# Kernel optimization log

Hardware: AMD Instinct MI355X
Metric: run time of the kernel (lower is better)

Reference implementation:

```python
import jax, jax.numpy as jnp
import numpy as np

EPS = 1e-5

def _ln(x, g, b):
    mu = x.mean(-1, keepdims=True)
    var = ((x - mu) ** 2).mean(-1, keepdims=True)
    return (x - mu) / jnp.sqrt(var + EPS) * g + b


def setup_inputs() -> dict:
    key = jax.random.key(0)
    B, Hd, Wd = 4, 32, 32
    C, heads = 1024, 16
    N = Hd * Wd
    pd = (C // 4) // 4  # DynamicPosBias pos_dim = 64
    hid = 4 * C
    ks = jax.random.split(key, 24)

    def w(k, shape):
        return jax.random.normal(k, shape, jnp.float32) * 0.02

    inp = {
        'x': jax.random.normal(ks[0], (B, N, C), jnp.float32),
        'norm1_g': jnp.ones((C,), jnp.float32), 'norm1_b': jnp.zeros((C,), jnp.float32),
        'q_w': w(ks[1], (C, C)),              # no bias (qkv_bias=False)
        'kv_w': w(ks[2], (C, 2 * C)),
        'proj_w': w(ks[3], (C, C)), 'proj_b': jnp.zeros((C,), jnp.float32),
        'pos_proj_w': w(ks[4], (2, pd)), 'pos_proj_b': jnp.zeros((pd,), jnp.float32),
        'ln1_g': jnp.ones((pd,), jnp.float32), 'ln1_b': jnp.zeros((pd,), jnp.float32),
        'lin1_w': w(ks[5], (pd, pd)), 'lin1_b': jnp.zeros((pd,), jnp.float32),
        'ln2_g': jnp.ones((pd,), jnp.float32), 'ln2_b': jnp.zeros((pd,), jnp.float32),
        'lin2_w': w(ks[6], (pd, pd)), 'lin2_b': jnp.zeros((pd,), jnp.float32),
        'ln3_g': jnp.ones((pd,), jnp.float32), 'ln3_b': jnp.zeros((pd,), jnp.float32),
        'lin3_w': w(ks[7], (pd, heads)), 'lin3_b': jnp.zeros((heads,), jnp.float32),
        'norm2_g': jnp.ones((C,), jnp.float32), 'norm2_b': jnp.zeros((C,), jnp.float32),
        'fc1_w': w(ks[8], (C, hid)), 'fc1_b': jnp.zeros((hid,), jnp.float32),
        'fc2_w': w(ks[9], (hid, C)), 'fc2_b': jnp.zeros((C,), jnp.float32),
        'H': Hd, 'W': Wd,
    }
    return inp


def _rel_pos(H, W):
    # coordinate offsets fed to the bias MLP: [(2H-1)(2W-1), 2]
    ph = np.arange(1 - H, H)
    pw = np.arange(1 - W, W)
    bh, bw = np.meshgrid(ph, pw, indexing='ij')
    biases = np.stack([bh.ravel(), bw.ravel()], axis=1).astype(np.float32)
    # relative position index: [HW, HW]
    ch, cw = np.meshgrid(np.arange(H), np.arange(W), indexing='ij')
    flat = np.stack([ch.ravel(), cw.ravel()])                 # [2, HW]
    rel = flat[:, :, None] - flat[:, None, :]                 # [2, HW, HW]
    rel = rel.transpose(1, 2, 0)
    rel[:, :, 0] += H - 1
    rel[:, :, 1] += W - 1
    rel[:, :, 0] *= 2 * W - 1
    idx = rel.sum(-1)                                         # [HW, HW]
    return jnp.asarray(biases), jnp.asarray(idx)


def reference(x, norm1_g, norm1_b, q_w, kv_w, proj_w, proj_b,
              pos_proj_w, pos_proj_b, ln1_g, ln1_b, lin1_w, lin1_b,
              ln2_g, ln2_b, lin2_w, lin2_b, ln3_g, ln3_b, lin3_w, lin3_b,
              norm2_g, norm2_b, fc1_w, fc1_b, fc2_w, fc2_b, H, W):
    B, N, C = x.shape
    heads = lin3_w.shape[1]
    d = C // heads
    scale = d ** (-0.5)

    # --- HLGAttention (stage_index==4: group_size=(H,W), h0_token=None) ---
    xn = _ln(x, norm1_g, norm1_b)
    q = (xn @ q_w).reshape(B, N, heads, d).transpose(0, 2, 1, 3)   # [B,h,N,d]
    kv = (xn @ kv_w).reshape(B, N, 2, heads, d)
    k = kv[:, :, 0].transpose(0, 2, 1, 3)                          # [B,h,N,d]
    v = kv[:, :, 1].transpose(0, 2, 1, 3)
    attn = jnp.einsum('bhnd,bhmd->bhnm', q, k) * scale

    # dynamic relative position bias via small MLP + gather
    biases, rel_idx = _rel_pos(H, W)
    pos = biases @ pos_proj_w + pos_proj_b
    pos = jax.nn.relu(_ln(pos, ln1_g, ln1_b)) @ lin1_w + lin1_b
    pos = jax.nn.relu(_ln(pos, ln2_g, ln2_b)) @ lin2_w + lin2_b
    pos = jax.nn.relu(_ln(pos, ln3_g, ln3_b)) @ lin3_w + lin3_b    # [(2H-1)(2W-1), heads]
    rpb = pos[rel_idx]                                              # [N,N,heads]
    attn = attn + rpb.transpose(2, 0, 1)[None]

    attn = jax.nn.softmax(attn, axis=-1)
    out = jnp.einsum('bhnm,bhmd->bhnd', attn, v)
    out = out.transpose(0, 2, 1, 3).reshape(B, N, C)
    out = out @ proj_w + proj_b
    x = x + out

    # --- MLP block ---
    h = _ln(x, norm2_g, norm2_b) @ fc1_w + fc1_b
    h = jax.nn.gelu(h, approximate=False)
    x = x + (h @ fc2_w + fc2_b)
    return x
```

## Files before the change

kernel.cpp:

```cpp
#include <hip/hip_runtime.h>
#include <cstdint>
#include <cstddef>

typedef __attribute__((ext_vector_type(8))) __bf16 bf16x8;
typedef __attribute__((ext_vector_type(8))) unsigned short us8;
typedef __attribute__((ext_vector_type(4))) unsigned short us4;
typedef __attribute__((ext_vector_type(4))) float f32x4;
typedef __attribute__((ext_vector_type(16))) float f32x16;

#define DEVI static __device__ __forceinline__

DEVI unsigned short f2bf(float f) {
  union { float f; unsigned u; } v; v.f = f;
  unsigned r = v.u + 0x7fffu + ((v.u >> 16) & 1u);
  return (unsigned short)(r >> 16);
}

DEVI f32x4 mfma16(us8 a, us8 b, f32x4 c) {
  return __builtin_amdgcn_mfma_f32_16x16x32_bf16(
      __builtin_bit_cast(bf16x8, a), __builtin_bit_cast(bf16x8, b), c, 0, 0, 0);
}

DEVI f32x16 mfma32(us8 a, us8 b, f32x16 c) {
  return __builtin_amdgcn_mfma_f32_32x32x16_bf16(
      __builtin_bit_cast(bf16x8, a), __builtin_bit_cast(bf16x8, b), c, 0, 0, 0);
}

DEVI f32x4 fzero4() { f32x4 v = {0.f, 0.f, 0.f, 0.f}; return v; }

DEVI float gelu_f(float v) {
  float z = 0.7978845608f * v * (1.f + 0.044715f * v * v);
  float e = __expf(2.f * z);
  float r = 1.f / (e + 1.f);
  return v * (1.f - r);
}

DEVI unsigned pkbf(float lo, float hi) {
  unsigned r;
  asm("v_cvt_pk_bf16_f32 %0, %1, %2" : "=v"(r) : "v"(lo), "v"(hi));
  return r;
}

DEVI void pswap(unsigned& x, unsigned& y) {
  asm volatile("v_permlane32_swap_b32 %0, %1" : "+v"(x), "+v"(y));
}

DEVI void gload16(const unsigned short* g, unsigned short* l) {
  __builtin_amdgcn_global_load_lds(
      (const __attribute__((address_space(1))) unsigned int*)g,
      (__attribute__((address_space(3))) unsigned int*)l, 16, 0, 0);
}

__global__ __launch_bounds__(256)
void transpose_w(const float* __restrict__ w, unsigned short* __restrict__ wt,
                 int K, int N) {
  __shared__ unsigned short tile[64][65];
  const int t = threadIdx.x;
  const int kb = blockIdx.x * 64, nb = blockIdx.y * 64;
#pragma unroll
  for (int i = 0; i < 4; ++i) {
    int r = i * 16 + (t >> 4);
    int c = (t & 15) * 4;
    float4 v = *(const float4*)(w + (size_t)(kb + r) * N + nb + c);
    tile[r][c + 0] = f2bf(v.x);
    tile[r][c + 1] = f2bf(v.y);
    tile[r][c + 2] = f2bf(v.z);
    tile[r][c + 3] = f2bf(v.w);
  }
  __syncthreads();
#pragma unroll
  for (int i = 0; i < 4; ++i) {
    int n = i * 16 + (t >> 4);
    int k = (t & 15) * 4;
    us4 o;
    o[0] = tile[k + 0][n];
    o[1] = tile[k + 1][n];
    o[2] = tile[k + 2][n];
    o[3] = tile[k + 3][n];
    *(us4*)(wt + (size_t)(nb + n) * K + kb + k) = o;
  }
}

__global__ __launch_bounds__(256)
void ln_kernel(const float* __restrict__ x, const float* __restrict__ g,
               const float* __restrict__ b, unsigned short* __restrict__ o) {
  const int row = blockIdx.x;
  const int tid = threadIdx.x;
  const float* xr = x + (size_t)row * 1024;
  float4 v = *(const float4*)(xr + tid * 4);
  float s = v.x + v.y + v.z + v.w;
  float sq = v.x * v.x + v.y * v.y + v.z * v.z + v.w * v.w;
#pragma unroll
  for (int m = 1; m < 64; m <<= 1) {
    s += __shfl_xor(s, m, 64);
    sq += __shfl_xor(sq, m, 64);
  }
  __shared__ float ss[4], ssq[4];
  const int wid = tid >> 6, lane = tid & 63;
  if (lane == 0) { ss[wid] = s; ssq[wid] = sq; }
  __syncthreads();
  s = ss[0] + ss[1] + ss[2] + ss[3];
  sq = ssq[0] + ssq[1] + ssq[2] + ssq[3];
  const float mu = s * (1.f / 1024.f);
  const float var = sq * (1.f / 1024.f) - mu * mu;
  const float rstd = rsqrtf(var + 1e-5f);
  const int c = tid * 4;
  float4 gv = *(const float4*)(g + c);
  float4 bv = *(const float4*)(b + c);
  us4 ov;
  ov[0] = f2bf((v.x - mu) * rstd * gv.x + bv.x);
  ov[1] = f2bf((v.y - mu) * rstd * gv.y + bv.y);
  ov[2] = f2bf((v.z - mu) * rstd * gv.z + bv.z);
  ov[3] = f2bf((v.w - mu) * rstd * gv.w + bv.w);
  *(us4*)(o + (size_t)row * 1024 + c) = ov;
}

DEVI float pos_layer(float p, const float* __restrict__ g,
                     const float* __restrict__ be, const float* __restrict__ w,
                     const float* __restrict__ bb, int lane) {
  float s = p, sq = p * p;
#pragma unroll
  for (int m = 1; m < 64; m <<= 1) {
    s += __shfl_xor(s, m, 64);
    sq += __shfl_xor(sq, m, 64);
  }
  float mu = s * (1.f / 64.f);
  float var = sq * (1.f / 64.f) - mu * mu;
  float rstd = rsqrtf(var + 1e-5f);
  float y = fmaxf((p - mu) * rstd * g[lane] + be[lane], 0.f);
  float o = bb[lane];
  for (int k = 0; k < 64; ++k) {
    float yk = __shfl(y, k, 64);
    o += yk * w[k * 64 + lane];
  }
  return o;
}

__global__ __launch_bounds__(256)
void pos_mlp(const float* __restrict__ pp_w, const float* __restrict__ pp_b,
             const float* __restrict__ g1, const float* __restrict__ b1,
             const float* __restrict__ w1, const float* __restrict__ bb1,
             const float* __restrict__ g2, const float* __restrict__ b2,
             const float* __restrict__ w2, const float* __restrict__ bb2,
             const float* __restrict__ g3, const float* __restrict__ b3,
             const float* __restrict__ w3, const float* __restrict__ bb3,
             float* __restrict__ posT) {
  const int wid = threadIdx.x >> 6, lane = threadIdx.x & 63;
  const int row = blockIdx.x * 4 + wid;
  if (row >= 3969) return;
  const float bh = (float)(row / 63) - 31.f;
  const float bw = (float)(row % 63) - 31.f;
  float p = bh * pp_w[lane] + bw * pp_w[64 + lane] + pp_b[lane];
  p = pos_layer(p, g1, b1, w1, bb1, lane);
  p = pos_layer(p, g2, b2, w2, bb2, lane);
  float s = p, sq = p * p;
#pragma unroll
  for (int m = 1; m < 64; m <<= 1) {
    s += __shfl_xor(s, m, 64);
    sq += __shfl_xor(sq, m, 64);
  }
  float mu = s * (1.f / 64.f);
  float var = sq * (1.f / 64.f) - mu * mu;
  float rstd = rsqrtf(var + 1e-5f);
  float y = fmaxf((p - mu) * rstd * g3[lane] + b3[lane], 0.f);
  float o = 0.f;
  for (int k = 0; k < 64; ++k) {
    float yk = __shfl(y, k, 64);
    o += yk * w3[k * 16 + (lane & 15)];
  }
  if (lane < 16) posT[(size_t)lane * 3969 + row] = o + bb3[lane];
}

template <int BM, int BN, bool HAS_BIAS, bool GELU_, bool HAS_RES,
          bool OUT_BF16, bool OUT_F32>
__global__ __launch_bounds__(256)
void gemm_bt(const unsigned short* __restrict__ A,
             const unsigned short* __restrict__ Bt,
             const float* __restrict__ bias, const float* __restrict__ res,
             unsigned short* __restrict__ outb, float* __restrict__ outf,
             int M, int N, int K) {
  constexpr int MT = BM / 32;
  constexpr int NT = BN / 32;
  __shared__ unsigned short As[BM * 128];
  __shared__ unsigned short Bs[BN * 128];
  const int tid = threadIdx.x;
  const int lane = tid & 63;
  const int wid = tid >> 6;
  const int lr = lane & 15, lg = lane >> 4;
  const int wr = wid >> 1, wc = wid & 1;
  const int brow = blockIdx.x, bcol = blockIdx.y;

  f32x4 acc[MT][NT];
#pragma unroll
  for (int mt = 0; mt < MT; ++mt)
#pragma unroll
    for (int nt = 0; nt < NT; ++nt) acc[mt][nt] = fzero4();

  const int sr = wid * 4 + (lane >> 4);
  const int sc = ((lane & 15) ^ ((sr & 7) << 1)) * 8;
  const unsigned short* Ag = A + (size_t)(brow * BM + sr) * K + sc;
  const unsigned short* Bg = Bt + (size_t)(bcol * BN + sr) * K + sc;

  const int nkb = K >> 7;
  for (int kb = 0; kb < nkb; ++kb) {
    __syncthreads();
#pragma unroll
    for (int q = 0; q < BM / 16; ++q)
      gload16(Ag + (size_t)(q * 16) * K + kb * 128,
              As + (q * 16 + wid * 4) * 128);
#pragma unroll
    for (int q = 0; q < BN / 16; ++q)
      gload16(Bg + (size_t)(q * 16) * K + kb * 128,
              Bs + (q * 16 + wid * 4) * 128);
    __syncthreads();
#pragma unroll
    for (int ks = 0; ks < 4; ++ks) {
      us8 af[MT], bfr[NT];
#pragma unroll
      for (int mt = 0; mt < MT; ++mt) {
        const int r = wr * (BM / 2) + mt * 16 + lr;
        const int ck = (ks * 4 + lg) ^ ((r & 7) << 1);
        af[mt] = *(const us8*)((const char*)As + r * 256 + ck * 16);
      }
#pragma unroll
      for (int nt = 0; nt < NT; ++nt) {
        const int r = wc * (BN / 2) + nt * 16 + lr;
        const int ck = (ks * 4 + lg) ^ ((r & 7) << 1);
        bfr[nt] = *(const us8*)((const char*)Bs + r * 256 + ck * 16);
      }
      __builtin_amdgcn_s_setprio(1);
#pragma unroll
      for (int mt = 0; mt < MT; ++mt)
#pragma unroll
        for (int nt = 0; nt < NT; ++nt)
          acc[mt][nt] = mfma16(af[mt], bfr[nt], acc[mt][nt]);
      __builtin_amdgcn_s_setprio(0);
    }
  }

#pragma unroll
  for (int mt = 0; mt < MT; ++mt) {
    const int row = brow * BM + wr * (BM / 2) + mt * 16 + 4 * lg;
#pragma unroll
    for (int nt = 0; nt < NT; ++nt) {
      const int col = bcol * BN + wc * (BN / 2) + nt * 16 + lr;
      float bsv = 0.f;
      if constexpr (HAS_BIAS) bsv = bias[col];
#pragma unroll
      for (int i = 0; i < 4; ++i) {
        float v = acc[mt][nt][i] + bsv;
        if constexpr (GELU_) v = gelu_f(v);
        if constexpr (HAS_RES) v += res[(size_t)(row + i) * N + col];
        if constexpr (OUT_F32) outf[(size_t)(row + i) * N + col] = v;
        if constexpr (OUT_BF16) outb[(size_t)(row + i) * N + col] = f2bf(v);
      }
    }
  }
}

__global__ __launch_bounds__(256)
void attn_kernel(const unsigned short* __restrict__ qkv,
                 const float* __restrict__ posT,
                 unsigned short* __restrict__ attnb) {
  __shared__ unsigned short Ks[64 * 64];
  __shared__ unsigned short Vt[64 * 64];

  const int tid = threadIdx.x;
  const int wid = tid >> 6;
  const int lane = tid & 63;
  const int ql = lane & 31;
  const int hi = lane >> 5;

  const int p = blockIdx.x;
  const int orig = (p & 7) * 64 + (p >> 3);
  const int b = orig >> 7;
  const int h = (orig >> 3) & 15;
  const int qt = orig & 7;

  const int LDQ = 3072;
  const int qg = qt * 128 + wid * 32 + ql;

  us8 qf[4];
  const unsigned short* qptr =
      qkv + (size_t)(b * 1024 + qg) * LDQ + h * 64 + 8 * hi;
#pragma unroll
  for (int db = 0; db < 4; ++db) qf[db] = *(const us8*)(qptr + db * 16);

  const float* pb = posT + (size_t)h * 3969;
  const int rb_q = ((qg >> 5) + 31) * 63 + (qg & 31) + 31 - 4 * hi;

  f32x16 oacc[2];
#pragma unroll
  for (int r = 0; r < 16; ++r) { oacc[0][r] = 0.f; oacc[1][r] = 0.f; }
  float mreg = -1e30f, lsum = 0.f;

  const int ksr = tid >> 2;
  const int ksc = (tid & 3) * 16;
  const int vk0 = (tid >> 4) * 4;
  const int vd0 = (tid & 15) * 4;

  const unsigned short* kbase = qkv + (size_t)(b * 1024) * LDQ + 1024 + h * 64;
  const unsigned short* vbase = qkv + (size_t)(b * 1024) * LDQ + 2048 + h * 64;

  us8 pk0 = *(const us8*)(kbase + (size_t)ksr * LDQ + ksc);
  us8 pk1 = *(const us8*)(kbase + (size_t)ksr * LDQ + ksc + 8);
  us4 pvv[4];
#pragma unroll
  for (int j = 0; j < 4; ++j)
    pvv[j] = *(const us4*)(vbase + (size_t)(vk0 + j) * LDQ + vd0);

  for (int kt = 0; kt < 16; ++kt) {
    __syncthreads();
    {
      char* ksb = (char*)Ks;
      const int swr = (ksr & 7) << 4;
      *(us8*)(ksb + ksr * 128 + ((ksc * 2) ^ swr)) = pk0;
      *(us8*)(ksb + ksr * 128 + (((ksc + 8) * 2) ^ swr)) = pk1;
      char* vtb = (char*)Vt;
#pragma unroll
      for (int u = 0; u < 4; ++u) {
        us4 w;
        w[0] = pvv[0][u]; w[1] = pvv[1][u]; w[2] = pvv[2][u]; w[3] = pvv[3][u];
        const int d = vd0 + u;
        *(us4*)(vtb + d * 128 + ((vk0 * 2) ^ ((d & 7) << 4))) = w;
      }
    }
    __syncthreads();

    if (kt < 15) {
      const unsigned short* kb2 = kbase + (size_t)((kt + 1) * 64) * LDQ;
      const unsigned short* vb2 = vbase + (size_t)((kt + 1) * 64) * LDQ;
      pk0 = *(const us8*)(kb2 + (size_t)ksr * LDQ + ksc);
      pk1 = *(const us8*)(kb2 + (size_t)ksr * LDQ + ksc + 8);
#pragma unroll
      for (int j = 0; j < 4; ++j)
        pvv[j] = *(const us4*)(vb2 + (size_t)(vk0 + j) * LDQ + vd0);
    }

    f32x16 st0, st1;
#pragma unroll
    for (int r = 0; r < 16; ++r) { st0[r] = 0.f; st1[r] = 0.f; }
    const char* ksb = (const char*)Ks;
    const int kswz = (ql & 7) << 4;
    __builtin_amdgcn_s_setprio(1);
#pragma unroll
    for (int db = 0; db < 4; ++db) {
      const int coff = (db * 32 + 16 * hi) ^ kswz;
      us8 kf0 = *(const us8*)(ksb + ql * 128 + coff);
      us8 kf1 = *(const us8*)(ksb + (32 + ql) * 128 + coff);
      st0 = mfma32(kf0, qf[db], st0);
      st1 = mfma32(kf1, qf[db], st1);
    }
    __builtin_amdgcn_s_setprio(0);

    float sv0[16], sv1[16];
    const float* pb0 = pb + (rb_q - 63 * (2 * kt));
    const float* pb1 = pb0 - 63;
    float mm[16];
#pragma unroll
    for (int r = 0; r < 16; ++r) {
      const int roff = (r & 3) + 8 * (r >> 2);
      float a = st0[r] * 0.125f + pb0[-roff];
      float c = st1[r] * 0.125f + pb1[-roff];
      sv0[r] = a;
      sv1[r] = c;
      mm[r] = fmaxf(a, c);
    }
#pragma unroll
    for (int w = 8; w >= 1; w >>= 1)
#pragma unroll
      for (int r = 0; r < w; ++r) mm[r] = fmaxf(mm[r], mm[r + w]);
    float mx = fmaxf(mreg, mm[0]);
    mx = fmaxf(mx, __shfl_xor(mx, 32, 64));
    const float f = __expf(mreg - mx);
    mreg = mx;

    float ts[16];
#pragma unroll
    for (int r = 0; r < 16; ++r) {
      float e0 = __expf(sv0[r] - mx);
      float e1 = __expf(sv1[r] - mx);
      sv0[r] = e0;
      sv1[r] = e1;
      ts[r] = e0 + e1;
    }
#pragma unroll
    for (int w = 8; w >= 1; w >>= 1)
#pragma unroll
      for (int r = 0; r < w; ++r) ts[r] += ts[r + w];
    lsum = lsum * f + ts[0];
#pragma unroll
    for (int r = 0; r < 16; ++r) { oacc[0][r] *= f; oacc[1][r] *= f; }

    const char* vtb = (const char*)Vt;
    auto pvfrag = [&](const float* sv, int kb) {
      const int B0 = (kb & 1) * 8;
      unsigned a0 = pkbf(sv[B0 + 0], sv[B0 + 1]);
      unsigned a1 = pkbf(sv[B0 + 2], sv[B0 + 3]);
      unsigned b0 = pkbf(sv[B0 + 4], sv[B0 + 5]);
      unsigned b1 = pkbf(sv[B0 + 6], sv[B0 + 7]);
      pswap(a0, b0);
      pswap(a1, b1);
      union { us8 s; unsigned u[4]; } fu;
      fu.u[0] = a0; fu.u[1] = a1; fu.u[2] = b0; fu.u[3] = b1;
      const int coff = (kb * 32 + 16 * hi) ^ kswz;
      us8 vf0 = *(const us8*)(vtb + ql * 128 + coff);
      us8 vf1 = *(const us8*)(vtb + (32 + ql) * 128 + coff);
      __builtin_amdgcn_s_setprio(1);
      oacc[0] = mfma32(vf0, fu.s, oacc[0]);
      oacc[1] = mfma32(vf1, fu.s, oacc[1]);
      __builtin_amdgcn_s_setprio(0);
    };
    pvfrag(sv0, 0);
    pvfrag(sv0, 1);
    pvfrag(sv1, 2);
    pvfrag(sv1, 3);
  }

  lsum += __shfl_xor(lsum, 32, 64);
  const float inv = 1.f / lsum;
  unsigned short* orow = attnb + (size_t)(b * 1024 + qg) * 1024 + h * 64;
#pragma unroll
  for (int dm = 0; dm < 2; ++dm)
#pragma unroll
    for (int r = 0; r < 16; ++r) {
      const int d = dm * 32 + (r & 3) + 8 * (r >> 2) + 4 * hi;
      orow[d] = f2bf(oacc[dm][r] * inv);
    }
}

extern "C" void kernel_launch(void* const* d_in, const int* in_sizes, int n_in,
                              void* d_out, int out_size, void* d_ws,
                              size_t ws_size, hipStream_t stream) {
  const float* x = (const float*)d_in[0];
  const float* n1g = (const float*)d_in[1];
  const float* n1b = (const float*)d_in[2];
  const float* q_w = (const float*)d_in[3];
  const float* kv_w = (const float*)d_in[4];
  const float* proj_w = (const float*)d_in[5];
  const float* proj_b = (const float*)d_in[6];
  const float* pp_w = (const float*)d_in[7];
  const float* pp_b = (const float*)d_in[8];
  const float* ln1g = (const float*)d_in[9];
  const float* ln1b = (const float*)d_in[10];
  const float* lin1w = (const float*)d_in[11];
  const float* lin1b = (const float*)d_in[12];
  const float* ln2g = (const float*)d_in[13];
  const float* ln2b = (const float*)d_in[14];
  const float* lin2w = (const float*)d_in[15];
  const float* lin2b = (const float*)d_in[16];
  const float* ln3g = (const float*)d_in[17];
  const float* ln3b = (const float*)d_in[18];
  const float* lin3w = (const float*)d_in[19];
  const float* lin3b = (const float*)d_in[20];
  const float* n2g = (const float*)d_in[21];
  const float* n2b = (const float*)d_in[22];
  const float* fc1_w = (const float*)d_in[23];
  const float* fc1_b = (const float*)d_in[24];
  const float* fc2_w = (const float*)d_in[25];
  const float* fc2_b = (const float*)d_in[26];
  float* out = (float*)d_out;

  char* ws = (char*)d_ws;
  const size_t MB = 1024ull * 1024ull;
  unsigned short* qkvT = (unsigned short*)(ws + 0 * MB);
  unsigned short* projT = (unsigned short*)(ws + 6 * MB);
  unsigned short* fc1T = (unsigned short*)(ws + 8 * MB);
  unsigned short* fc2T = (unsigned short*)(ws + 16 * MB);
  unsigned short* xn = (unsigned short*)(ws + 24 * MB);
  unsigned short* qkv = (unsigned short*)(ws + 32 * MB);
  unsigned short* attnb = (unsigned short*)(ws + 56 * MB);
  float* x1 = (float*)(ws + 64 * MB);
  unsigned short* x2n = (unsigned short*)(ws + 80 * MB);
  unsigned short* hb = (unsigned short*)(ws + 88 * MB);
  float* posT = (float*)(ws + 120 * MB);

  transpose_w<<<dim3(16, 16), 256, 0, stream>>>(q_w, qkvT, 1024, 1024);
  transpose_w<<<dim3(16, 32), 256, 0, stream>>>(
      kv_w, qkvT + (size_t)1024 * 1024, 1024, 2048);
  transpose_w<<<dim3(16, 16), 256, 0, stream>>>(proj_w, projT, 1024, 1024);
  transpose_w<<<dim3(16, 64), 256, 0, stream>>>(fc1_w, fc1T, 1024, 4096);
  transpose_w<<<dim3(64, 16), 256, 0, stream>>>(fc2_w, fc2T, 4096, 1024);

  ln_kernel<<<4096, 256, 0, stream>>>(x, n1g, n1b, xn);
  pos_mlp<<<993, 256, 0, stream>>>(pp_w, pp_b, ln1g, ln1b, lin1w, lin1b, ln2g,
                                   ln2b, lin2w, lin2b, ln3g, ln3b, lin3w,
                                   lin3b, posT);

  gemm_bt<128, 128, false, false, false, true, false>
      <<<dim3(32, 24), 256, 0, stream>>>(xn, qkvT, nullptr, nullptr, qkv,
                                         nullptr, 4096, 3072, 1024);

  attn_kernel<<<512, 256, 0, stream>>>(qkv, posT, attnb);

  gemm_bt<64, 128, true, false, true, false, true>
      <<<dim3(64, 8), 256, 0, stream>>>(attnb, projT, proj_b, x, nullptr, x1,
                                        4096, 1024, 1024);

  ln_kernel<<<4096, 256, 0, stream>>>(x1, n2g, n2b, x2n);

  gemm_bt<128, 128, true, true, false, true, false>
      <<<dim3(32, 32), 256, 0, stream>>>(x2n, fc1T, fc1_b, nullptr, hb,
                                         nullptr, 4096, 4096, 1024);

  gemm_bt<64, 128, true, false, true, false, true>
      <<<dim3(64, 8), 256, 0, stream>>>(hb, fc2T, fc2_b, x1, nullptr, out,
                                        4096, 1024, 4096);

  (void)in_sizes; (void)n_in; (void)out_size; (void)ws_size;
}
```

Measured before the change: 239.7 us.

## Fuse prep kernels, halve attention block size, add lazy softmax rescaling

Merges the five weight-transpose launches, the first LayerNorm and the position-bias MLP into a single block-indexed prep kernel, removing several kernel launches. The attention kernel now uses 128-thread blocks covering 64 query rows each, launched as 1024 blocks with wider per-thread K/V staging loads. Online softmax now rescales the accumulator only when the new row max exceeds the running max by more than 8, which skips exp and multiply work but lets unnormalised exponentials grow up to e^8.

After: 223.4 us, median of 2. 1.07x faster.

```diff
diff --git a/kernel.cpp b/kernel.cpp
--- a/kernel.cpp
+++ b/kernel.cpp
@@ -51,12 +51,11 @@
       (__attribute__((address_space(3))) unsigned int*)l, 16, 0, 0);
 }
 
-__global__ __launch_bounds__(256)
-void transpose_w(const float* __restrict__ w, unsigned short* __restrict__ wt,
-                 int K, int N) {
-  __shared__ unsigned short tile[64][65];
+DEVI void transpose_body(const float* __restrict__ w,
+                         unsigned short* __restrict__ wt, int K, int N,
+                         int kbi, int nbi, unsigned short (*tile)[65]) {
   const int t = threadIdx.x;
-  const int kb = blockIdx.x * 64, nb = blockIdx.y * 64;
+  const int kb = kbi * 64, nb = nbi * 64;
 #pragma unroll
   for (int i = 0; i < 4; ++i) {
     int r = i * 16 + (t >> 4);
@@ -78,6 +77,123 @@
     o[2] = tile[k + 2][n];
     o[3] = tile[k + 3][n];
     *(us4*)(wt + (size_t)(nb + n) * K + kb + k) = o;
+  }
+}
+
+DEVI float pos_layer(float p, const float* __restrict__ g,
+                     const float* __restrict__ be, const float* __restrict__ w,
+                     const float* __restrict__ bb, int lane) {
+  float s = p, sq = p * p;
+#pragma unroll
+  for (int m = 1; m < 64; m <<= 1) {
+    s += __shfl_xor(s, m, 64);
+    sq += __shfl_xor(sq, m, 64);
+  }
+  float mu = s * (1.f / 64.f);
+  float var = sq * (1.f / 64.f) - mu * mu;
+  float rstd = rsqrtf(var + 1e-5f);
+  float y = fmaxf((p - mu) * rstd * g[lane] + be[lane], 0.f);
+  float o = bb[lane];
+  for (int k = 0; k < 64; ++k) {
+    float yk = __shfl(y, k, 64);
+    o += yk * w[k * 64 + lane];
+  }
+  return o;
+}
+
+__global__ __launch_bounds__(256)
+void prep_kernel(const float* __restrict__ x, const float* __restrict__ n1g,
+                 const float* __restrict__ n1b, unsigned short* __restrict__ xn,
+                 const float* __restrict__ q_w, const float* __restrict__ kv_w,
+                 const float* __restrict__ proj_w,
+                 const float* __restrict__ fc1_w,
+                 const float* __restrict__ fc2_w,
+                 unsigned short* __restrict__ qkvT,
+                 unsigned short* __restrict__ projT,
+                 unsigned short* __restrict__ fc1T,
+                 unsigned short* __restrict__ fc2T,
+                 const float* __restrict__ pp_w, const float* __restrict__ pp_b,
+                 const float* __restrict__ g1, const float* __restrict__ b1,
+                 const float* __restrict__ w1, const float* __restrict__ bb1,
+                 const float* __restrict__ g2, const float* __restrict__ b2,
+                 const float* __restrict__ w2, const float* __restrict__ bb2,
+                 const float* __restrict__ g3, const float* __restrict__ b3,
+                 const float* __restrict__ w3, const float* __restrict__ bb3,
+                 float* __restrict__ posT) {
+  __shared__ unsigned short tile[64][65];
+  __shared__ float ss[4], ssq[4];
+  const int blk = blockIdx.x;
+  const int tid = threadIdx.x;
+
+  if (blk < 4096) {
+    const int row = blk;
+    const float* xr = x + (size_t)row * 1024;
+    float4 v = *(const float4*)(xr + tid * 4);
+    float s = v.x + v.y + v.z + v.w;
+    float sq = v.x * v.x + v.y * v.y + v.z * v.z + v.w * v.w;
+#pragma unroll
+    for (int m = 1; m < 64; m <<= 1) {
+      s += __shfl_xor(s, m, 64);
+      sq += __shfl_xor(sq, m, 64);
+    }
+    const int wid = tid >> 6, lane = tid & 63;
+    if (lane == 0) { ss[wid] = s; ssq[wid] = sq; }
+    __syncthreads();
+    s = ss[0] + ss[1] + ss[2] + ss[3];
+    sq = ssq[0] + ssq[1] + ssq[2] + ssq[3];
+    const float mu = s * (1.f / 1024.f);
+    const float var = sq * (1.f / 1024.f) - mu * mu;
+    const float rstd = rsqrtf(var + 1e-5f);
+    const int c = tid * 4;
+    float4 gv = *(const float4*)(n1g + c);
+    float4 bv = *(const float4*)(n1b + c);
+    us4 ov;
+    ov[0] = f2bf((v.x - mu) * rstd * gv.x + bv.x);
+    ov[1] = f2bf((v.y - mu) * rstd * gv.y + bv.y);
+    ov[2] = f2bf((v.z - mu) * rstd * gv.z + bv.z);
+    ov[3] = f2bf((v.w - mu) * rstd * gv.w + bv.w);
+    *(us4*)(xn + (size_t)row * 1024 + c) = ov;
+  } else if (blk < 5089) {
+    const int wid = tid >> 6, lane = tid & 63;
+    const int row = (blk - 4096) * 4 + wid;
+    if (row >= 3969) return;
+    const float bh = (float)(row / 63) - 31.f;
+    const float bw = (float)(row % 63) - 31.f;
+    float p = bh * pp_w[lane] + bw * pp_w[64 + lane] + pp_b[lane];
+    p = pos_layer(p, g1, b1, w1, bb1, lane);
+    p = pos_layer(p, g2, b2, w2, bb2, lane);
+    float s = p, sq = p * p;
+#pragma unroll
+    for (int m = 1; m < 64; m <<= 1) {
+      s += __shfl_xor(s, m, 64);
+      sq += __shfl_xor(sq, m, 64);
+    }
+    float mu = s * (1.f / 64.f);
+    float var = sq * (1.f / 64.f) - mu * mu;
+    float rstd = rsqrtf(var + 1e-5f);
+    float y = fmaxf((p - mu) * rstd * g3[lane] + b3[lane], 0.f);
+    float o = 0.f;
+    for (int k = 0; k < 64; ++k) {
+      float yk = __shfl(y, k, 64);
+      o += yk * w3[k * 16 + (lane & 15)];
+    }
+    if (lane < 16) posT[(size_t)lane * 3969 + row] = o + bb3[lane];
+  } else if (blk < 5345) {
+    const int lin = blk - 5089;
+    transpose_body(q_w, qkvT, 1024, 1024, lin & 15, lin >> 4, tile);
+  } else if (blk < 5857) {
+    const int lin = blk - 5345;
+    transpose_body(kv_w, qkvT + (size_t)1024 * 1024, 1024, 2048, lin & 15,
+                   lin >> 4, tile);
+  } else if (blk < 6113) {
+    const int lin = blk - 5857;
+    transpose_body(proj_w, projT, 1024, 1024, lin & 15, lin >> 4, tile);
+  } else if (blk < 7137) {
+    const int lin = blk - 6113;
+    transpose_body(fc1_w, fc1T, 1024, 4096, lin & 15, lin >> 4, tile);
+  } else {
+    const int lin = blk - 7137;
+    transpose_body(fc2_w, fc2T, 4096, 1024, lin & 63, lin >> 6, tile);
   }
 }
 
@@ -115,62 +231,6 @@
   *(us4*)(o + (size_t)row * 1024 + c) = ov;
 }
 
-DEVI float pos_layer(float p, const float* __restrict__ g,
-                     const float* __restrict__ be, const float* __restrict__ w,
-                     const float* __restrict__ bb, int lane) {
-  float s = p, sq = p * p;
-#pragma unroll
-  for (int m = 1; m < 64; m <<= 1) {
-    s += __shfl_xor(s, m, 64);
-    sq += __shfl_xor(sq, m, 64);
-  }
-  float mu = s * (1.f / 64.f);
-  float var = sq * (1.f / 64.f) - mu * mu;
-  float rstd = rsqrtf(var + 1e-5f);
-  float y = fmaxf((p - mu) * rstd * g[lane] + be[lane], 0.f);
-  float o = bb[lane];
-  for (int k = 0; k < 64; ++k) {
-    float yk = __shfl(y, k, 64);
-    o += yk * w[k * 64 + lane];
-  }
-  return o;
-}
-
-__global__ __launch_bounds__(256)
-void pos_mlp(const float* __restrict__ pp_w, const float* __restrict__ pp_b,
-             const float* __restrict__ g1, const float* __restrict__ b1,
-             const float* __restrict__ w1, const float* __restrict__ bb1,
-             const float* __restrict__ g2, const float* __restrict__ b2,
-             const float* __restrict__ w2, const float* __restrict__ bb2,
-             const float* __restrict__ g3, const float* __restrict__ b3,
-             const float* __restrict__ w3, const float* __restrict__ bb3,
-             float* __restrict__ posT) {
-  const int wid = threadIdx.x >> 6, lane = threadIdx.x & 63;
-  const int row = blockIdx.x * 4 + wid;
-  if (row >= 3969) return;
-  const float bh = (float)(row / 63) - 31.f;
-  const float bw = (float)(row % 63) - 31.f;
-  float p = bh * pp_w[lane] + bw * pp_w[64 + lane] + pp_b[lane];
-  p = pos_layer(p, g1, b1, w1, bb1, lane);
-  p = pos_layer(p, g2, b2, w2, bb2, lane);
-  float s = p, sq = p * p;
-#pragma unroll
-  for (int m = 1; m < 64; m <<= 1) {
-    s += __shfl_xor(s, m, 64);
-    sq += __shfl_xor(sq, m, 64);
-  }
-  float mu = s * (1.f / 64.f);
-  float var = sq * (1.f / 64.f) - mu * mu;
-  float rstd = rsqrtf(var + 1e-5f);
-  float y = fmaxf((p - mu) * rstd * g3[lane] + b3[lane], 0.f);
-  float o = 0.f;
-  for (int k = 0; k < 64; ++k) {
-    float yk = __shfl(y, k, 64);
-    o += yk * w3[k * 16 + (lane & 15)];
-  }
-  if (lane < 16) posT[(size_t)lane * 3969 + row] = o + bb3[lane];
-}
-
 template <int BM, int BN, bool HAS_BIAS, bool GELU_, bool HAS_RES,
           bool OUT_BF16, bool OUT_F32>
 __global__ __launch_bounds__(256)
@@ -258,7 +318,7 @@
   }
 }
 
-__global__ __launch_bounds__(256)
+__global__ __launch_bounds__(128)
 void attn_kernel(const unsigned short* __restrict__ qkv,
                  const float* __restrict__ posT,
                  unsigned short* __restrict__ attnb) {
@@ -272,13 +332,13 @@
   const int hi = lane >> 5;
 
   const int p = blockIdx.x;
-  const int orig = (p & 7) * 64 + (p >> 3);
-  const int b = orig >> 7;
-  const int h = (orig >> 3) & 15;
-  const int qt = orig & 7;
+  const int orig = (p & 7) * 128 + (p >> 3);
+  const int b = orig >> 8;
+  const int h = (orig >> 4) & 15;
+  const int qt = orig & 15;
 
   const int LDQ = 3072;
-  const int qg = qt * 128 + wid * 32 + ql;
+  const int qg = qt * 64 + wid * 32 + ql;
 
   us8 qf[4];
   const unsigned short* qptr =
@@ -294,19 +354,21 @@
   for (int r = 0; r < 16; ++r) { oacc[0][r] = 0.f; oacc[1][r] = 0.f; }
   float mreg = -1e30f, lsum = 0.f;
 
-  const int ksr = tid >> 2;
-  const int ksc = (tid & 3) * 16;
-  const int vk0 = (tid >> 4) * 4;
+  const int ksr = tid >> 1;
+  const int ksc = (tid & 1) * 32;
   const int vd0 = (tid & 15) * 4;
+  const int vk0 = (tid >> 4) * 8;
 
   const unsigned short* kbase = qkv + (size_t)(b * 1024) * LDQ + 1024 + h * 64;
   const unsigned short* vbase = qkv + (size_t)(b * 1024) * LDQ + 2048 + h * 64;
 
-  us8 pk0 = *(const us8*)(kbase + (size_t)ksr * LDQ + ksc);
-  us8 pk1 = *(const us8*)(kbase + (size_t)ksr * LDQ + ksc + 8);
-  us4 pvv[4];
+  us8 pk[4];
+  us4 pvv[8];
 #pragma unroll
   for (int j = 0; j < 4; ++j)
+    pk[j] = *(const us8*)(kbase + (size_t)ksr * LDQ + ksc + j * 8);
+#pragma unroll
+  for (int j = 0; j < 8; ++j)
     pvv[j] = *(const us4*)(vbase + (size_t)(vk0 + j) * LDQ + vd0);
 
   for (int kt = 0; kt < 16; ++kt) {
@@ -314,15 +376,20 @@
     {
       char* ksb = (char*)Ks;
       const int swr = (ksr & 7) << 4;
-      *(us8*)(ksb + ksr * 128 + ((ksc * 2) ^ swr)) = pk0;
-      *(us8*)(ksb + ksr * 128 + (((ksc + 8) * 2) ^ swr)) = pk1;
+#pragma unroll
+      for (int j = 0; j < 4; ++j)
+        *(us8*)(ksb + ksr * 128 + (((ksc + j * 8) * 2) ^ swr)) = pk[j];
       char* vtb = (char*)Vt;
+      const int cbase = vk0 << 1;
 #pragma unroll
       for (int u = 0; u < 4; ++u) {
-        us4 w;
-        w[0] = pvv[0][u]; w[1] = pvv[1][u]; w[2] = pvv[2][u]; w[3] = pvv[3][u];
         const int d = vd0 + u;
-        *(us4*)(vtb + d * 128 + ((vk0 * 2) ^ ((d & 7) << 4))) = w;
+        const int addr = d * 128 + (cbase ^ ((d & 7) << 4));
+        us4 lo, hi4;
+        lo[0] = pvv[0][u]; lo[1] = pvv[1][u]; lo[2] = pvv[2][u]; lo[3] = pvv[3][u];
+        hi4[0] = pvv[4][u]; hi4[1] = pvv[5][u]; hi4[2] = pvv[6][u]; hi4[3] = pvv[7][u];
+        *(us4*)(vtb + addr) = lo;
+        *(us4*)(vtb + addr + 8) = hi4;
       }
     }
     __syncthreads();
@@ -330,10 +397,11 @@
     if (kt < 15) {
       const unsigned short* kb2 = kbase + (size_t)((kt + 1) * 64) * LDQ;
       const unsigned short* vb2 = vbase + (size_t)((kt + 1) * 64) * LDQ;
-      pk0 = *(const us8*)(kb2 + (size_t)ksr * LDQ + ksc);
-      pk1 = *(const us8*)(kb2 + (size_t)ksr * LDQ + ksc + 8);
 #pragma unroll
       for (int j = 0; j < 4; ++j)
+        pk[j] = *(const us8*)(kb2 + (size_t)ksr * LDQ + ksc + j * 8);
+#pragma unroll
+      for (int j = 0; j < 8; ++j)
         pvv[j] = *(const us4*)(vb2 + (size_t)(vk0 + j) * LDQ + vd0);
     }
 
@@ -370,16 +438,21 @@
     for (int w = 8; w >= 1; w >>= 1)
 #pragma unroll
       for (int r = 0; r < w; ++r) mm[r] = fmaxf(mm[r], mm[r + w]);
-    float mx = fmaxf(mreg, mm[0]);
-    mx = fmaxf(mx, __shfl_xor(mx, 32, 64));
-    const float f = __expf(mreg - mx);
-    mreg = mx;
+    float pm = fmaxf(mm[0], __shfl_xor(mm[0], 32, 64));
+
+    if (pm > mreg + 8.f) {
+      const float f = __expf(mreg - pm);
+      lsum *= f;
+#pragma unroll
+      for (int r = 0; r < 16; ++r) { oacc[0][r] *= f; oacc[1][r] *= f; }
+      mreg = pm;
+    }
 
     float ts[16];
 #pragma unroll
     for (int r = 0; r < 16; ++r) {
-      float e0 = __expf(sv0[r] - mx);
-      float e1 = __expf(sv1[r] - mx);
+      float e0 = __expf(sv0[r] - mreg);
+      float e1 = __expf(sv1[r] - mreg);
       sv0[r] = e0;
       sv1[r] = e1;
       ts[r] = e0 + e1;
@@ -388,9 +461,7 @@
     for (int w = 8; w >= 1; w >>= 1)
 #pragma unroll
       for (int r = 0; r < w; ++r) ts[r] += ts[r + w];
-    lsum = lsum * f + ts[0];
-#pragma unroll
-    for (int r = 0; r < 16; ++r) { oacc[0][r] *= f; oacc[1][r] *= f; }
+    lsum += ts[0];
 
     const char* vtb = (const char*)Vt;
     auto pvfrag = [&](const float* sv, int kb) {
@@ -475,23 +546,16 @@
   unsigned short* hb = (unsigned short*)(ws + 88 * MB);
   float* posT = (float*)(ws + 120 * MB);
 
-  transpose_w<<<dim3(16, 16), 256, 0, stream>>>(q_w, qkvT, 1024, 1024);
-  transpose_w<<<dim3(16, 32), 256, 0, stream>>>(
-      kv_w, qkvT + (size_t)1024 * 1024, 1024, 2048);
-  transpose_w<<<dim3(16, 16), 256, 0, stream>>>(proj_w, projT, 1024, 1024);
-  transpose_w<<<dim3(16, 64), 256, 0, stream>>>(fc1_w, fc1T, 1024, 4096);
-  transpose_w<<<dim3(64, 16), 256, 0, stream>>>(fc2_w, fc2T, 4096, 1024);
-
-  ln_kernel<<<4096, 256, 0, stream>>>(x, n1g, n1b, xn);
-  pos_mlp<<<993, 256, 0, stream>>>(pp_w, pp_b, ln1g, ln1b, lin1w, lin1b, ln2g,
-                                   ln2b, lin2w, lin2b, ln3g, ln3b, lin3w,
-                                   lin3b, posT);
+  prep_kernel<<<8161, 256, 0, stream>>>(
+      x, n1g, n1b, xn, q_w, kv_w, proj_w, fc1_w, fc2_w, qkvT, projT, fc1T,
+      fc2T, pp_w, pp_b, ln1g, ln1b, lin1w, lin1b, ln2g, ln2b, lin2w, lin2b,
+      ln3g, ln3b, lin3w, lin3b, posT);
 
   gemm_bt<128, 128, false, false, false, true, false>
       <<<dim3(32, 24), 256, 0, stream>>>(xn, qkvT, nullptr, nullptr, qkv,
                                          nullptr, 4096, 3072, 1024);
 
-  attn_kernel<<<512, 256, 0, stream>>>(qkv, posT, attnb);
+  attn_kernel<<<1024, 128, 0, stream>>>(qkv, posT, attnb);
 
   gemm_bt<64, 128, true, false, true, false, true>
       <<<dim3(64, 8), 256, 0, stream>>>(attnb, projT, proj_b, x, nullptr, x1,
```
